# Kernel tuning notes

Hardware: AMD Instinct MI355X
Metric: run time of the kernel (lower is better)

The kernel has to match this reference:

```python
import jax, jax.numpy as jnp
import numpy as np

HEAD = 16
HEAD_DIM = 64
DIM = 1024
NEG = -1000000000.0


def setup_inputs() -> dict:
    key = jax.random.key(0)
    ks = jax.random.split(key, 8)
    B, S = 4, 2048
    s = 0.02
    return {
        "Q": jax.random.normal(ks[0], (B, S, DIM), dtype=jnp.float32),
        "K": jax.random.normal(ks[1], (B, S, DIM), dtype=jnp.float32),
        "V": jax.random.normal(ks[2], (B, S, DIM), dtype=jnp.float32),
        "Wq": jax.random.normal(ks[3], (HEAD * HEAD_DIM, DIM), dtype=jnp.float32) * s,
        "Wk": jax.random.normal(ks[4], (HEAD * HEAD_DIM, DIM), dtype=jnp.float32) * s,
        "Wv": jax.random.normal(ks[5], (HEAD * HEAD_DIM, DIM), dtype=jnp.float32) * s,
        "Wo": jax.random.normal(ks[6], (DIM, HEAD * HEAD_DIM), dtype=jnp.float32) * s,
        "bo": jax.random.normal(ks[7], (DIM,), dtype=jnp.float32) * s,
    }


def reference(Q, K, V, Wq, Wk, Wv, Wo, bo):
    B, S, _ = Q.shape
    # projections (nn.Linear: x @ W^T), split heads -> (b, h, t, d)
    def proj(x, W):
        return (x @ W.T).reshape(B, S, HEAD, HEAD_DIM).transpose(0, 2, 1, 3)
    q = proj(Q, Wq)
    k = proj(K, Wk)
    v = proj(V, Wv)
    scores = jnp.einsum("bhqd,bhkd->bhqk", q, k) / jnp.sqrt(jnp.float32(HEAD_DIM))
    causal = jnp.tril(jnp.ones((S, S), dtype=bool))
    scores = jnp.where(causal, scores, NEG)
    weights = jax.nn.softmax(scores, axis=-1)
    out = jnp.einsum("bhqk,bhkd->bhqd", weights, v)
    out = out.transpose(0, 2, 1, 3).reshape(B, S, HEAD * HEAD_DIM)
    out = out @ Wo.T + bo
    return out, weights
```

## Files before the change

kernel.cpp:

```cpp
#include <hip/hip_runtime.h>
#include <hip/hip_bf16.h>

typedef __hip_bfloat16 bf16;
typedef __attribute__((ext_vector_type(8))) short bf16x8;
typedef __attribute__((ext_vector_type(4))) float f32x4;

#define HEADS 16
#define HDIM  64
#define DIM   1024
#define SEQ   2048
#define BATCH 4
#define BS    (BATCH * SEQ)
#define SCALE 0.125f

#define MFMA16(a, b, c) __builtin_amdgcn_mfma_f32_16x16x32_bf16(a, b, c, 0, 0, 0)

__device__ __forceinline__ void gload_lds16(const void* g, void* l) {
    __builtin_amdgcn_global_load_lds(
        (const __attribute__((address_space(1))) void*)g,
        (__attribute__((address_space(3))) void*)l, 16, 0, 0);
}

__device__ __forceinline__ void cvt8(const float* __restrict__ src, bf16* __restrict__ dst,
                                     size_t i)
{
    float4 f0 = *(const float4*)&src[i];
    float4 f1 = *(const float4*)&src[i + 4];
    union { bf16 h[8]; uint4 u; } pk;
    pk.h[0] = __float2bfloat16(f0.x); pk.h[1] = __float2bfloat16(f0.y);
    pk.h[2] = __float2bfloat16(f0.z); pk.h[3] = __float2bfloat16(f0.w);
    pk.h[4] = __float2bfloat16(f1.x); pk.h[5] = __float2bfloat16(f1.y);
    pk.h[6] = __float2bfloat16(f1.z); pk.h[7] = __float2bfloat16(f1.w);
    *(uint4*)&dst[i] = pk.u;
}

__global__ __launch_bounds__(256) void cvt_kernel(
    const float* __restrict__ Q, const float* __restrict__ K, const float* __restrict__ V,
    const float* __restrict__ Wq, const float* __restrict__ Wk, const float* __restrict__ Wv,
    bf16* __restrict__ xq, bf16* __restrict__ xk, bf16* __restrict__ xv,
    bf16* __restrict__ wq, bf16* __restrict__ wk, bf16* __restrict__ wv)
{
    const int seg = blockIdx.y;
    const float* src; bf16* dst; size_t n;
    switch (seg) {
        case 0: src = Q;  dst = xq; n = (size_t)BS * DIM;   break;
        case 1: src = K;  dst = xk; n = (size_t)BS * DIM;   break;
        case 2: src = V;  dst = xv; n = (size_t)BS * DIM;   break;
        case 3: src = Wq; dst = wq; n = (size_t)DIM * DIM;  break;
        case 4: src = Wk; dst = wk; n = (size_t)DIM * DIM;  break;
        default: src = Wv; dst = wv; n = (size_t)DIM * DIM; break;
    }
    size_t i = ((size_t)blockIdx.x * 256 + threadIdx.x) * 8;
    if (i >= n) return;
    cvt8(src, dst, i);
}

__global__ __launch_bounds__(256) void cvt_wo_kernel(
    const float* __restrict__ Wo, bf16* __restrict__ wo)
{
    size_t i = ((size_t)blockIdx.x * 256 + threadIdx.x) * 8;
    cvt8(Wo, wo, i);
}

__device__ __forceinline__ void mfma_core_1024(
    const bf16* __restrict__ A, const bf16* __restrict__ B,
    int m0, int n0, bf16* sA, f32x4 acc[4][4])
{
    const int tid = threadIdx.x, lane = tid & 63, wave = tid >> 6;
    const int l15 = lane & 15, lg = lane >> 4;
    const int wr = wave >> 1, wc = wave & 1;
    bf16* sB = sA + 16 * 512;

    const bf16* gsrc = (wave < 2) ? A : B;
    const int   gm0  = (wave < 2) ? m0 : n0;
    bf16*       sdst = (wave < 2) ? sA : sB;
    const int   wv2  = wave & 1;

#define STAGE(k0_) { \
    _Pragma("unroll") for (int u = 0; u < 8; ++u) { \
        const int c = wv2 * 8 + u; \
        const int mg = c >> 1, s = c & 1; \
        gload_lds16(gsrc + (size_t)(gm0 + mg * 16 + l15) * DIM + (k0_) + s * 32 + lg * 8, \
                    sdst + c * 512); \
    } }

    STAGE(0);
#pragma unroll 1
    for (int t = 0; t < DIM / 64; ++t) {
        __syncthreads();
#pragma unroll
        for (int s = 0; s < 2; ++s) {
            bf16x8 af[4], bfr[4];
#pragma unroll
            for (int i = 0; i < 4; ++i)
                af[i] = *(const bf16x8*)(sA + ((wr * 4 + i) * 2 + s) * 512 + lane * 8);
#pragma unroll
            for (int j = 0; j < 4; ++j)
                bfr[j] = *(const bf16x8*)(sB + ((wc * 4 + j) * 2 + s) * 512 + lane * 8);
#pragma unroll
            for (int i = 0; i < 4; ++i)
#pragma unroll
                for (int j = 0; j < 4; ++j)
                    acc[i][j] = MFMA16(af[i], bfr[j], acc[i][j]);
        }
        __syncthreads();
        if (t < DIM / 64 - 1) STAGE((t + 1) * 64);
    }
#undef STAGE
}

__global__ __launch_bounds__(256) void proj_mfma_kernel(
    const bf16* __restrict__ Xq, const bf16* __restrict__ Xk, const bf16* __restrict__ Xv,
    const bf16* __restrict__ Wq, const bf16* __restrict__ Wk, const bf16* __restrict__ Wv,
    bf16* __restrict__ qo, bf16* __restrict__ ko, bf16* __restrict__ vo)
{
    __shared__ alignas(16) bf16 smem[16384];
    const int z = blockIdx.z;
    const bf16* X = z == 0 ? Xq : z == 1 ? Xk : Xv;
    const bf16* W = z == 0 ? Wq : z == 1 ? Wk : Wv;
    const int m0 = blockIdx.y * 128, n0 = blockIdx.x * 128;
    f32x4 acc[4][4] = {};
    mfma_core_1024(X, W, m0, n0, smem, acc);

    const int tid = threadIdx.x, lane = tid & 63, wave = tid >> 6;
    const int l15 = lane & 15, lg = lane >> 4, wr = wave >> 1, wc = wave & 1;
    const int h = blockIdx.x * 2 + wc;

    if (z != 2) {
        bf16* O = z == 0 ? qo : ko;
#pragma unroll
        for (int i = 0; i < 4; ++i)
#pragma unroll
            for (int r = 0; r < 4; ++r) {
                int m = m0 + wr * 64 + i * 16 + lg * 4 + r;
                int bb = m >> 11, ss = m & (SEQ - 1);
                size_t base = ((size_t)(bb * HEADS + h) * SEQ + ss) * HDIM;
#pragma unroll
                for (int j = 0; j < 4; ++j)
                    O[base + j * 16 + l15] = __float2bfloat16(acc[i][j][r]);
            }
    } else {
#pragma unroll
        for (int i = 0; i < 4; ++i) {
            int s0 = m0 + wr * 64 + i * 16 + lg * 4;
            int bb = s0 >> 11, ss = s0 & (SEQ - 1);
#pragma unroll
            for (int j = 0; j < 4; ++j) {
                int d = j * 16 + l15;
                union { bf16 h4[4]; uint2 u; } pk;
#pragma unroll
                for (int r = 0; r < 4; ++r) pk.h4[r] = __float2bfloat16(acc[i][j][r]);
                *(uint2*)&vo[((size_t)(bb * HEADS + h) * HDIM + d) * SEQ + ss] = pk.u;
            }
        }
    }
}

__global__ __launch_bounds__(256) void attn_kernel(
    const bf16* __restrict__ qws, const bf16* __restrict__ kws, const bf16* __restrict__ vtws,
    float* __restrict__ weights, bf16* __restrict__ attn_out)
{
    __shared__ alignas(16) bf16 Ks[4096];
    __shared__ alignas(16) bf16 Vs[4096];
    __shared__ alignas(16) bf16 Ps[4096];

    const int tid  = threadIdx.x;
    const int lane = tid & 63;
    const int wave = tid >> 6;
    const int l15  = lane & 15;
    const int lg   = lane >> 4;
    const int qt = blockIdx.x;
    const int h  = blockIdx.y, b = blockIdx.z;
    const int bh = b * HEADS + h;
    const int q0 = qt * 64;

    const bf16* qbase = qws + (size_t)bh * SEQ * HDIM;
    const bf16* kbase = kws + (size_t)bh * SEQ * HDIM;
    const bf16* vbase = vtws + (size_t)bh * HDIM * SEQ;

    bf16x8 qa0, qa1;
    {
        const bf16* qp = qbase + (size_t)(q0 + 16 * wave + l15) * HDIM + lg * 8;
        qa0 = *(const bf16x8*)qp;
        qa1 = *(const bf16x8*)(qp + 32);
    }

#define LOADK(kt_, r0, r1) { \
    const bf16* rp = kbase + (size_t)((kt_) * 64 + 16 * wave + l15) * HDIM + lg * 8; \
    r0 = *(const uint4*)rp; r1 = *(const uint4*)(rp + 32); }
#define STOREK(r0, r1) { \
    *(uint4*)&Ks[((wave * 2 + 0) * 64 + lane) * 8] = r0; \
    *(uint4*)&Ks[((wave * 2 + 1) * 64 + lane) * 8] = r1; }
#define LOADV(kt_, r0, r1) { \
    const bf16* rp = vbase + (size_t)(16 * wave + l15) * SEQ + (kt_) * 64 + lg * 8; \
    r0 = *(const uint4*)rp; r1 = *(const uint4*)(rp + 32); }
#define STOREV(r0, r1) { \
    *(uint4*)&Vs[((wave * 2 + 0) * 64 + lane) * 8] = r0; \
    *(uint4*)&Vs[((wave * 2 + 1) * 64 + lane) * 8] = r1; }
#define QKT(acc_) { \
    _Pragma("unroll") \
    for (int ct = 0; ct < 4; ++ct) { \
        bf16x8 b0 = *(const bf16x8*)&Ks[((ct * 2 + 0) * 64 + lane) * 8]; \
        bf16x8 b1 = *(const bf16x8*)&Ks[((ct * 2 + 1) * 64 + lane) * 8]; \
        acc_[ct] = MFMA16(qa0, b0, acc_[ct]); \
        acc_[ct] = MFMA16(qa1, b1, acc_[ct]); \
    } }

    float m_run[4] = {-1e30f, -1e30f, -1e30f, -1e30f};
    float l_run[4] = {0.f, 0.f, 0.f, 0.f};

    {
        uint4 k0, k1;
        LOADK(0, k0, k1);
        STOREK(k0, k1);
    }
    for (int kt = 0; kt <= qt; ++kt) {
        __syncthreads();
        f32x4 acc[4] = {};
        QKT(acc);
        const bool more = kt < qt;
        uint4 nk0, nk1;
        if (more) LOADK(kt + 1, nk0, nk1);
        const bool diag = (kt == qt);
#pragma unroll
        for (int r = 0; r < 4; ++r) {
            float s0 = acc[0][r] * SCALE;
            float s1 = acc[1][r] * SCALE;
            float s2 = acc[2][r] * SCALE;
            float s3 = acc[3][r] * SCALE;
            if (diag) {
                int rr = 16 * wave + lg * 4 + r;
                if (l15      > rr) s0 = -1e30f;
                if (l15 + 16 > rr) s1 = -1e30f;
                if (l15 + 32 > rr) s2 = -1e30f;
                if (l15 + 48 > rr) s3 = -1e30f;
            }
            float t = fmaxf(fmaxf(s0, s1), fmaxf(s2, s3));
            t = fmaxf(t, __shfl_xor(t, 1));
            t = fmaxf(t, __shfl_xor(t, 2));
            t = fmaxf(t, __shfl_xor(t, 4));
            t = fmaxf(t, __shfl_xor(t, 8));
            float mn = fmaxf(m_run[r], t);
            float ps = __expf(s0 - mn) + __expf(s1 - mn)
                     + __expf(s2 - mn) + __expf(s3 - mn);
            ps += __shfl_xor(ps, 1);
            ps += __shfl_xor(ps, 2);
            ps += __shfl_xor(ps, 4);
            ps += __shfl_xor(ps, 8);
            l_run[r] = l_run[r] * __expf(m_run[r] - mn) + ps;
            m_run[r] = mn;
        }
        __syncthreads();
        if (more) STOREK(nk0, nk1);
    }

    float il[4];
#pragma unroll
    for (int r = 0; r < 4; ++r) il[r] = 1.0f / l_run[r];

    {
        uint4 k0, k1, v0, v1;
        LOADK(0, k0, k1);
        LOADV(0, v0, v1);
        STOREK(k0, k1);
        STOREV(v0, v1);
    }
    f32x4 oacc[4] = {};
    size_t wbase[4];
#pragma unroll
    for (int r = 0; r < 4; ++r)
        wbase[r] = ((size_t)bh * SEQ + (q0 + 16 * wave + lg * 4 + r)) * SEQ;

    for (int kt = 0; kt <= qt; ++kt) {
        __syncthreads();
        f32x4 acc[4] = {};
        QKT(acc);
        const bool more = kt < qt;
        uint4 nk0, nk1, nv0, nv1;
        if (more) { LOADK(kt + 1, nk0, nk1); LOADV(kt + 1, nv0, nv1); }
        const bool diag = (kt == qt);
#pragma unroll
        for (int ct = 0; ct < 4; ++ct) {
#pragma unroll
            for (int r = 0; r < 4; ++r) {
                float s = acc[ct][r] * SCALE;
                if (diag && (ct * 16 + l15 > 16 * wave + lg * 4 + r)) s = -1e30f;
                float w = __expf(s - m_run[r]) * il[r];
                __builtin_nontemporal_store(
                    w, &weights[wbase[r] + kt * 64 + ct * 16 + l15]);
                Ps[((wave * 2 + (ct >> 1)) * 64
                    + (lg * 4 + r) + 16 * ((ct & 1) * 2 + (l15 >> 3))) * 8
                   + (l15 & 7)] = __float2bfloat16(w);
            }
        }
        bf16x8 pa0 = *(const bf16x8*)&Ps[((wave * 2 + 0) * 64 + lane) * 8];
        bf16x8 pa1 = *(const bf16x8*)&Ps[((wave * 2 + 1) * 64 + lane) * 8];
#pragma unroll
        for (int td = 0; td < 4; ++td) {
            bf16x8 vb0 = *(const bf16x8*)&Vs[((td * 2 + 0) * 64 + lane) * 8];
            bf16x8 vb1 = *(const bf16x8*)&Vs[((td * 2 + 1) * 64 + lane) * 8];
            oacc[td] = MFMA16(pa0, vb0, oacc[td]);
            oacc[td] = MFMA16(pa1, vb1, oacc[td]);
        }
        __syncthreads();
        if (more) { STOREK(nk0, nk1); STOREV(nv0, nv1); }
    }

#pragma unroll
    for (int td = 0; td < 4; ++td)
#pragma unroll
        for (int r = 0; r < 4; ++r) {
            int rowg = q0 + 16 * wave + lg * 4 + r;
            attn_out[((size_t)b * SEQ + rowg) * DIM + h * HDIM + td * 16 + l15]
                = __float2bfloat16(oacc[td][r]);
        }

    const int zc0 = (qt + 1) * 64;
    if (zc0 < SEQ) {
        const int nc4 = (SEQ - zc0) >> 2;
        const size_t base = ((size_t)bh * SEQ + q0) * SEQ + zc0;
        const f32x4 z = {0.f, 0.f, 0.f, 0.f};
        for (int r = 0; r < 64; ++r)
            for (int c = tid; c < nc4; c += 256)
                __builtin_nontemporal_store(
                    z, (f32x4*)&weights[base + (size_t)r * SEQ + (size_t)c * 4]);
    }
#undef LOADK
#undef STOREK
#undef LOADV
#undef STOREV
#undef QKT
}

__global__ __launch_bounds__(256) void oproj_mfma_kernel(
    const bf16* __restrict__ A, const bf16* __restrict__ Wo,
    const float* __restrict__ bo, float* __restrict__ out)
{
    __shared__ alignas(16) bf16 smem[16384];
    const int m0 = blockIdx.y * 128, n0 = blockIdx.x * 128;
    f32x4 acc[4][4] = {};
    mfma_core_1024(A, Wo, m0, n0, smem, acc);

    const int tid = threadIdx.x, lane = tid & 63, wave = tid >> 6;
    const int l15 = lane & 15, lg = lane >> 4, wr = wave >> 1, wc = wave & 1;
    float bv[4];
#pragma unroll
    for (int j = 0; j < 4; ++j) bv[j] = bo[n0 + wc * 64 + j * 16 + l15];
#pragma unroll
    for (int i = 0; i < 4; ++i)
#pragma unroll
        for (int r = 0; r < 4; ++r) {
            int m = m0 + wr * 64 + i * 16 + lg * 4 + r;
#pragma unroll
            for (int j = 0; j < 4; ++j)
                out[(size_t)m * DIM + n0 + wc * 64 + j * 16 + l15] = acc[i][j][r] + bv[j];
        }
}

extern "C" void kernel_launch(void* const* d_in, const int* in_sizes, int n_in,
                              void* d_out, int out_size, void* d_ws, size_t ws_size,
                              hipStream_t stream)
{
    const float* Q  = (const float*)d_in[0];
    const float* K  = (const float*)d_in[1];
    const float* V  = (const float*)d_in[2];
    const float* Wq = (const float*)d_in[3];
    const float* Wk = (const float*)d_in[4];
    const float* Wv = (const float*)d_in[5];
    const float* Wo = (const float*)d_in[6];
    const float* bo = (const float*)d_in[7];

    float* out     = (float*)d_out;
    float* weights = out + (size_t)BS * DIM;

    const size_t XN = (size_t)BS * DIM;
    const size_t WN = (size_t)DIM * DIM;
    const size_t scratch_elems = 3 * XN + 3 * WN;
    bf16* cvt = (bf16*)(weights + ((size_t)268435456 - scratch_elems / 2));
    bf16* xq  = cvt;
    bf16* xk  = xq + XN;
    bf16* xv  = xk + XN;
    bf16* wqc = xv + XN;
    bf16* wkc = wqc + WN;
    bf16* wvc = wkc + WN;

    bf16* qws  = (bf16*)d_ws;
    bf16* kws  = qws + (size_t)BS * DIM;
    bf16* vtws = kws + (size_t)BS * DIM;
    bf16* aws  = vtws + (size_t)BS * DIM;
    bf16* woc  = qws;

    dim3 blk(256);
    cvt_kernel<<<dim3(4096, 6), blk, 0, stream>>>(
        Q, K, V, Wq, Wk, Wv, xq, xk, xv, wqc, wkc, wvc);
    proj_mfma_kernel<<<dim3(DIM / 128, BS / 128, 3), blk, 0, stream>>>(
        xq, xk, xv, wqc, wkc, wvc, qws, kws, vtws);
    attn_kernel<<<dim3(SEQ / 64, HEADS, BATCH), blk, 0, stream>>>(
        qws, kws, vtws, weights, aws);
    cvt_wo_kernel<<<dim3(WN / (256 * 8)), blk, 0, stream>>>(Wo, woc);
    oproj_mfma_kernel<<<dim3(DIM / 128, BS / 128), blk, 0, stream>>>(
        aws, woc, bo, out);
}
```

Before: 504.5 us.

## Transpose QK^T MFMA output layout for vectorized weight stores and exp2 softmax

Swaps the MFMA operands so each lane holds four consecutive key columns of a single query row. This lets the attention-weight writes become 16-byte nontemporal vector stores, and the bf16 P tile is written to LDS in 8-byte chunks. The scale is folded into a log2e constant so the softmax uses the hardware exp2, and the row reductions drop to two cross-lane shuffles. Query tiles are launched in reverse order so the longest causal blocks start first. The risk is LDS bank conflicts in the new P layout, and the masking and index changes must stay correct.

```diff
diff --git a/kernel.cpp b/kernel.cpp
--- a/kernel.cpp
+++ b/kernel.cpp
@@ -12,7 +12,9 @@
 #define BATCH 4
 #define BS    (BATCH * SEQ)
 #define SCALE 0.125f
-
+#define CS    0.1803368801111f
+
+#define EXP2F(x) __builtin_amdgcn_exp2f(x)
 #define MFMA16(a, b, c) __builtin_amdgcn_mfma_f32_16x16x32_bf16(a, b, c, 0, 0, 0)
 
 __device__ __forceinline__ void gload_lds16(const void* g, void* l) {
@@ -169,10 +171,11 @@
     const int wave = tid >> 6;
     const int l15  = lane & 15;
     const int lg   = lane >> 4;
-    const int qt = blockIdx.x;
+    const int qt = (int)gridDim.x - 1 - (int)blockIdx.x;
     const int h  = blockIdx.y, b = blockIdx.z;
     const int bh = b * HEADS + h;
     const int q0 = qt * 64;
+    const int qloc = 16 * wave + l15;
 
     const bf16* qbase = qws + (size_t)bh * SEQ * HDIM;
     const bf16* kbase = kws + (size_t)bh * SEQ * HDIM;
@@ -180,7 +183,7 @@
 
     bf16x8 qa0, qa1;
     {
-        const bf16* qp = qbase + (size_t)(q0 + 16 * wave + l15) * HDIM + lg * 8;
+        const bf16* qp = qbase + (size_t)(q0 + qloc) * HDIM + lg * 8;
         qa0 = *(const bf16x8*)qp;
         qa1 = *(const bf16x8*)(qp + 32);
     }
@@ -202,12 +205,12 @@
     for (int ct = 0; ct < 4; ++ct) { \
         bf16x8 b0 = *(const bf16x8*)&Ks[((ct * 2 + 0) * 64 + lane) * 8]; \
         bf16x8 b1 = *(const bf16x8*)&Ks[((ct * 2 + 1) * 64 + lane) * 8]; \
-        acc_[ct] = MFMA16(qa0, b0, acc_[ct]); \
-        acc_[ct] = MFMA16(qa1, b1, acc_[ct]); \
+        acc_[ct] = MFMA16(b0, qa0, acc_[ct]); \
+        acc_[ct] = MFMA16(b1, qa1, acc_[ct]); \
     } }
 
-    float m_run[4] = {-1e30f, -1e30f, -1e30f, -1e30f};
-    float l_run[4] = {0.f, 0.f, 0.f, 0.f};
+    float m_run = -1e30f;
+    float l_run = 0.f;
 
     {
         uint4 k0, k1;
@@ -222,41 +225,37 @@
         uint4 nk0, nk1;
         if (more) LOADK(kt + 1, nk0, nk1);
         const bool diag = (kt == qt);
-#pragma unroll
-        for (int r = 0; r < 4; ++r) {
-            float s0 = acc[0][r] * SCALE;
-            float s1 = acc[1][r] * SCALE;
-            float s2 = acc[2][r] * SCALE;
-            float s3 = acc[3][r] * SCALE;
-            if (diag) {
-                int rr = 16 * wave + lg * 4 + r;
-                if (l15      > rr) s0 = -1e30f;
-                if (l15 + 16 > rr) s1 = -1e30f;
-                if (l15 + 32 > rr) s2 = -1e30f;
-                if (l15 + 48 > rr) s3 = -1e30f;
+        float t[4][4];
+#pragma unroll
+        for (int ct = 0; ct < 4; ++ct)
+#pragma unroll
+            for (int r = 0; r < 4; ++r) {
+                float v = acc[ct][r] * CS;
+                if (diag && (ct * 16 + lg * 4 + r > qloc)) v = -1e30f;
+                t[ct][r] = v;
             }
-            float t = fmaxf(fmaxf(s0, s1), fmaxf(s2, s3));
-            t = fmaxf(t, __shfl_xor(t, 1));
-            t = fmaxf(t, __shfl_xor(t, 2));
-            t = fmaxf(t, __shfl_xor(t, 4));
-            t = fmaxf(t, __shfl_xor(t, 8));
-            float mn = fmaxf(m_run[r], t);
-            float ps = __expf(s0 - mn) + __expf(s1 - mn)
-                     + __expf(s2 - mn) + __expf(s3 - mn);
-            ps += __shfl_xor(ps, 1);
-            ps += __shfl_xor(ps, 2);
-            ps += __shfl_xor(ps, 4);
-            ps += __shfl_xor(ps, 8);
-            l_run[r] = l_run[r] * __expf(m_run[r] - mn) + ps;
-            m_run[r] = mn;
-        }
+        float tm = -1e30f;
+#pragma unroll
+        for (int ct = 0; ct < 4; ++ct)
+#pragma unroll
+            for (int r = 0; r < 4; ++r) tm = fmaxf(tm, t[ct][r]);
+        tm = fmaxf(tm, __shfl_xor(tm, 16));
+        tm = fmaxf(tm, __shfl_xor(tm, 32));
+        float mn = fmaxf(m_run, tm);
+        float ps = 0.f;
+#pragma unroll
+        for (int ct = 0; ct < 4; ++ct)
+#pragma unroll
+            for (int r = 0; r < 4; ++r) ps += EXP2F(t[ct][r] - mn);
+        ps += __shfl_xor(ps, 16);
+        ps += __shfl_xor(ps, 32);
+        l_run = l_run * EXP2F(m_run - mn) + ps;
+        m_run = mn;
         __syncthreads();
         if (more) STOREK(nk0, nk1);
     }
 
-    float il[4];
-#pragma unroll
-    for (int r = 0; r < 4; ++r) il[r] = 1.0f / l_run[r];
+    const float il = 1.0f / l_run;
 
     {
         uint4 k0, k1, v0, v1;
@@ -266,10 +265,7 @@
         STOREV(v0, v1);
     }
     f32x4 oacc[4] = {};
-    size_t wbase[4];
-#pragma unroll
-    for (int r = 0; r < 4; ++r)
-        wbase[r] = ((size_t)bh * SEQ + (q0 + 16 * wave + lg * 4 + r)) * SEQ;
+    const size_t wrow = ((size_t)bh * SEQ + q0 + qloc) * SEQ;
 
     for (int kt = 0; kt <= qt; ++kt) {
         __syncthreads();
@@ -281,17 +277,21 @@
         const bool diag = (kt == qt);
 #pragma unroll
         for (int ct = 0; ct < 4; ++ct) {
+            f32x4 w4;
+            union { bf16 h4[4]; uint2 u; } pk;
 #pragma unroll
             for (int r = 0; r < 4; ++r) {
-                float s = acc[ct][r] * SCALE;
-                if (diag && (ct * 16 + l15 > 16 * wave + lg * 4 + r)) s = -1e30f;
-                float w = __expf(s - m_run[r]) * il[r];
-                __builtin_nontemporal_store(
-                    w, &weights[wbase[r] + kt * 64 + ct * 16 + l15]);
-                Ps[((wave * 2 + (ct >> 1)) * 64
-                    + (lg * 4 + r) + 16 * ((ct & 1) * 2 + (l15 >> 3))) * 8
-                   + (l15 & 7)] = __float2bfloat16(w);
+                float v = acc[ct][r] * CS;
+                if (diag && (ct * 16 + lg * 4 + r > qloc)) v = -1e30f;
+                float w = EXP2F(v - m_run) * il;
+                w4[r] = w;
+                pk.h4[r] = __float2bfloat16(w);
             }
+            __builtin_nontemporal_store(
+                w4, (f32x4*)&weights[wrow + kt * 64 + ct * 16 + lg * 4]);
+            *(uint2*)&Ps[(((wave * 2 + (ct >> 1)) * 64
+                           + ((ct & 1) * 2 + (lg >> 1)) * 16 + l15) * 8
+                          + (lg & 1) * 4)] = pk.u;
         }
         bf16x8 pa0 = *(const bf16x8*)&Ps[((wave * 2 + 0) * 64 + lane) * 8];
         bf16x8 pa1 = *(const bf16x8*)&Ps[((wave * 2 + 1) * 64 + lane) * 8];
```

Measured after the change: 484.0 us. 4.1% less time.
